# Kernel optimization log

Measured on AMD Instinct MI355X. Metric: run time of the kernel, lower is better.

The kernel has to match this reference:

```python
import jax, jax.numpy as jnp
import numpy as np

N_HEADS, D_K, D_MODEL = 16, 64, 1024
B, S = 2, 2048


def setup_inputs() -> dict:
    key = jax.random.key(0)
    ks = jax.random.split(key, 9)
    scale = 1.0 / np.sqrt(D_MODEL)
    cscale = 1.0 / np.sqrt(N_HEADS * D_K)
    return {
        "x": jax.random.normal(ks[0], (B, S, D_MODEL), dtype=jnp.float32),
        # per-head projection weights, stacked over heads: [H, d_model, d_k]
        "Wq": jax.random.uniform(ks[1], (N_HEADS, D_MODEL, D_K), jnp.float32, -scale, scale),
        "bq": jax.random.uniform(ks[2], (N_HEADS, D_K), jnp.float32, -scale, scale),
        "Wk": jax.random.uniform(ks[3], (N_HEADS, D_MODEL, D_K), jnp.float32, -scale, scale),
        "bk": jax.random.uniform(ks[4], (N_HEADS, D_K), jnp.float32, -scale, scale),
        "Wv": jax.random.uniform(ks[5], (N_HEADS, D_MODEL, D_K), jnp.float32, -scale, scale),
        "bv": jax.random.uniform(ks[6], (N_HEADS, D_K), jnp.float32, -scale, scale),
        # concat projection: [H*d_k, d_model]
        "Wc": jax.random.uniform(ks[7], (N_HEADS * D_K, D_MODEL), jnp.float32, -cscale, cscale),
        "bc": jax.random.uniform(ks[8], (D_MODEL,), jnp.float32, -cscale, cscale),
    }


def reference(x, Wq, bq, Wk, bk, Wv, bv, Wc, bc):
    # Per-head projections, vectorized across heads: [B,H,S,d_k]
    q = jnp.einsum("bsd,hdk->bhsk", x, Wq) + bq[None, :, None, :]
    k = jnp.einsum("bsd,hdk->bhsk", x, Wk) + bk[None, :, None, :]
    v = jnp.einsum("bsd,hdk->bhsk", x, Wv) + bv[None, :, None, :]
    # scores: [B,H,Sq,Skv]
    scores = jnp.einsum("bhsk,bhtk->bhst", q, k) / jnp.sqrt(jnp.asarray(D_K, x.dtype))
    # FAITHFUL to original: softmax over dim=1 of [B,S,S] = the QUERY axis (axis 2 here)
    attn = jax.nn.softmax(scores, axis=2)
    out = jnp.einsum("bhst,bhtk->bhsk", attn, v)  # [B,H,S,d_k]
    # concat heads along feature dim: [B,S,H*d_k]
    cat = jnp.transpose(out, (0, 2, 1, 3)).reshape(x.shape[0], x.shape[1], -1)
    return cat @ Wc + bc
```

## Files before the change

kernel.cpp:

```cpp
#include <hip/hip_runtime.h>
#include <hip/hip_bf16.h>

#define NH 16
#define DK 64
#define DM 1024
#define BB 2
#define SS 2048
#define BS (BB*SS)

typedef __attribute__((ext_vector_type(8))) short bf16x8;
typedef __attribute__((ext_vector_type(4))) short short4v;
typedef __attribute__((ext_vector_type(4))) float f32x4;

#define MFMA16 __builtin_amdgcn_mfma_f32_16x16x32_bf16

#if __has_builtin(__builtin_amdgcn_exp2f)
#define EXP2(x) __builtin_amdgcn_exp2f(x)
#else
#define EXP2(x) __expf((x) * 0.6931471805599453f)
#endif

static __device__ __forceinline__ float bf2f(short s) {
  union { unsigned u; float f; } v;
  v.u = ((unsigned)(unsigned short)s) << 16;
  return v.f;
}
static __device__ __forceinline__ short f2bf(float f) {
  union { float f; unsigned u; } v; v.f = f;
  unsigned r = (v.u + 0x7fffu + ((v.u >> 16) & 1u)) >> 16;
  return (short)r;
}
static __device__ __forceinline__ unsigned pkbf(float a, float b) {
  __hip_bfloat162 h = __float22bfloat162_rn(make_float2(a, b));
  union { __hip_bfloat162 h; unsigned u; } c; c.h = h; return c.u;
}

template<int C16>
static __device__ __forceinline__ int soff(int row, int chunk) {
  return row*(C16*8) + ((chunk ^ (row & (C16-1))) << 3);
}

template<int C16, int R>
static __device__ __forceinline__ void stage(const short* __restrict__ g, int gstride,
                                             short* l, int wave, int lane) {
  const int rloc = lane / C16;
  const int c    = lane % C16;
#pragma unroll
  for (int rr = 0; rr < R; rr += 4*(64/C16)) {
    int rbase = rr + wave*(64/C16);
    int row   = rbase + rloc;
    int cg    = c ^ (row & (C16-1));
    __builtin_amdgcn_global_load_lds(
        (const __attribute__((address_space(1))) void*)(g + (size_t)row*gstride + cg*8),
        (__attribute__((address_space(3))) void*)(l + rbase*(C16*8)),
        16, 0, 0);
  }
}

static __device__ __forceinline__ int permK(int r) {
  return ((r >> 5) << 5) | ((((r >> 2) & 3)) << 3) | (((r >> 4) & 1) << 2) | (r & 3);
}
template<int R>
static __device__ __forceinline__ void stageP(const short* __restrict__ g, int gstride,
                                              short* l, int wave, int lane) {
  const int rloc = lane >> 3;
  const int c    = lane & 7;
#pragma unroll
  for (int rr = 0; rr < R; rr += 32) {
    int rbase = rr + wave*8;
    int row   = rbase + rloc;
    int cg    = c ^ (row & 7);
    __builtin_amdgcn_global_load_lds(
        (const __attribute__((address_space(1))) void*)(g + (size_t)permK(row)*gstride + cg*8),
        (__attribute__((address_space(3))) void*)(l + rbase*64),
        16, 0, 0);
  }
}

__global__ __launch_bounds__(256) void k_convert(
    const float* __restrict__ x,
    const float* __restrict__ Wq, const float* __restrict__ Wk,
    const float* __restrict__ Wv, const float* __restrict__ Wc,
    short* __restrict__ xb, short* __restrict__ Wt, short* __restrict__ Wct) {
  __shared__ float T[64][65];
  const int tid = threadIdx.x;
  int bx = blockIdx.x;
  const int XB = BS*DM/(256*4);
  if (bx < XB) {
    int i = (bx*256 + tid)*4;
    float4 v = *(const float4*)&x[i];
    union { unsigned u[2]; short4v s; } o;
    o.u[0] = pkbf(v.x, v.y); o.u[1] = pkbf(v.z, v.w);
    *(short4v*)&xb[i] = o.s;
    return;
  }
  bx -= XB;
  if (bx < 48*16) {
    int th = bx >> 4, d0 = (bx & 15) * 64;
    int type = th >> 4, h = th & 15;
    const float* W = ((type == 0) ? Wq : (type == 1) ? Wk : Wv)
                     + (size_t)h*DM*DK + (size_t)d0*DK;
#pragma unroll
    for (int p = 0; p < 4; p++) {
      int dr = p*16 + (tid >> 4), dkc = (tid & 15) * 4;
      float4 v = *(const float4*)&W[(size_t)dr*DK + dkc];
      T[dkc+0][dr]=v.x; T[dkc+1][dr]=v.y; T[dkc+2][dr]=v.z; T[dkc+3][dr]=v.w;
    }
    __syncthreads();
#pragma unroll
    for (int e = 0; e < 2; e++) {
      int c = tid*2 + e, dk = c >> 3, dd = (c & 7) * 8;
      union { short s[8]; int4 v; } u;
#pragma unroll
      for (int j = 0; j < 8; j++) u.s[j] = f2bf(T[dk][dd+j]);
      *(int4*)&Wt[((size_t)th*DK + dk)*DM + d0 + dd] = u.v;
    }
    return;
  }
  bx -= 48*16;
  int n0 = (bx >> 4) * 64, k0 = (bx & 15) * 64;
#pragma unroll
  for (int p = 0; p < 4; p++) {
    int kr = p*16 + (tid >> 4), nc = (tid & 15) * 4;
    float4 v = *(const float4*)&Wc[(size_t)(k0+kr)*DM + n0 + nc];
    T[nc+0][kr]=v.x; T[nc+1][kr]=v.y; T[nc+2][kr]=v.z; T[nc+3][kr]=v.w;
  }
  __syncthreads();
#pragma unroll
  for (int e = 0; e < 2; e++) {
    int c = tid*2 + e, n = c >> 3, kk = (c & 7) * 8;
    union { short s[8]; int4 v; } u;
#pragma unroll
    for (int j = 0; j < 8; j++) u.s[j] = f2bf(T[n][kk+j]);
    *(int4*)&Wct[(size_t)(n0+n)*DM + k0 + kk] = u.v;
  }
}

__global__ __launch_bounds__(256) void k_qkv(
    const short* __restrict__ xb, const short* __restrict__ Wt,
    const float* __restrict__ bq, const float* __restrict__ bk,
    const float* __restrict__ bv,
    short* __restrict__ Qb, short* __restrict__ Kb, short* __restrict__ Vb) {
  __shared__ __align__(16) short smem[128*130];
  short* As = smem;
  short* Bs = smem + 8192;
  const int tid = threadIdx.x, wave = tid >> 6, lane = tid & 63;
  const int l15 = lane & 15, quad = lane >> 4;
  const int id = blockIdx.x, xcd = id & 7, j = id >> 3;
  const int m0 = (xcd*4 + (j & 3)) * 128, n0 = (j >> 2) * 128;
  const int mw = (wave & 1) * 64, nw = (wave >> 1) * 64;
  f32x4 acc[4][4] = {};
  for (int k0 = 0; k0 < DM; k0 += 64) {
    stage<8,128>(xb + (size_t)m0*DM + k0, DM, As, wave, lane);
    stage<8,128>(Wt + (size_t)n0*DM + k0, DM, Bs, wave, lane);
    __syncthreads();
#pragma unroll
    for (int ks = 0; ks < 2; ks++) {
      bf16x8 a[4], b[4];
#pragma unroll
      for (int g = 0; g < 4; g++)  a[g]  = *(const bf16x8*)&As[soff<8>(mw + g*16 + l15,  ks*4 + quad)];
#pragma unroll
      for (int nf = 0; nf < 4; nf++) b[nf] = *(const bf16x8*)&Bs[soff<8>(nw + nf*16 + l15, ks*4 + quad)];
#pragma unroll
      for (int g = 0; g < 4; g++)
#pragma unroll
        for (int nf = 0; nf < 4; nf++)
          acc[g][nf] = MFMA16(a[g], b[nf], acc[g][nf], 0, 0, 0);
    }
    __syncthreads();
  }
  const int th = (n0 + nw) >> 6;
  const int type = th >> 4, h = th & 15;
  const float* bias = ((type == 0) ? bq : (type == 1) ? bk : bv) + h*DK;
  const float scale = (type == 0) ? 0.18033688011112042f : 1.0f;
#pragma unroll
  for (int nf = 0; nf < 4; nf++) {
    float bval = bias[nf*16 + l15];
#pragma unroll
    for (int g = 0; g < 4; g++)
#pragma unroll
      for (int r = 0; r < 4; r++)
        smem[(mw + g*16 + quad*4 + r)*130 + nw + nf*16 + l15] =
            f2bf((acc[g][nf][r] + bval) * scale);
  }
  __syncthreads();
  const int row = tid >> 1, half = tid & 1;
  const int th2 = (n0 >> 6) + half;
  const int type2 = th2 >> 4, h2 = th2 & 15;
  short* dst = (type2 == 0) ? Qb : (type2 == 1) ? Kb : Vb;
  const int m = m0 + row, b_ = m >> 11, s = m & (SS-1);
  short* drow = dst + (size_t)((b_*NH + h2)*SS + s)*DK;
  const short* crow = smem + row*130 + half*64;
#pragma unroll
  for (int c8 = 0; c8 < 8; c8++)
    *(int4*)&drow[c8*8] = *(const int4*)&crow[c8*8];
}

__global__ __launch_bounds__(256) void k_stats(
    const short* __restrict__ Qb, const short* __restrict__ Kb,
    const short* __restrict__ Vb, short* __restrict__ Vt) {
  __shared__ __align__(16) short smem[3*8192];
  __shared__ float red[4][64];
  __shared__ float zinv[128];
  short* Ks = smem;
  const int tid = threadIdx.x, wave = tid >> 6, lane = tid & 63;
  const int l15 = lane & 15, quad = lane >> 4;
  const int id = blockIdx.x, xcd = id & 7, j = id >> 3;
  const int bh = xcd*4 + (j & 3), t0 = (j >> 2) * 128;
  const short* Qg = Qb + (size_t)bh * SS * DK;
  const short* Kg = Kb + (size_t)bh * SS * DK;
  const int mw = (wave & 1) * 64, nw = (wave >> 1) * 64;
  stage<8,128>(Kg + (size_t)t0*DK, DK, Ks, wave, lane);
  stage<8,128>(Qg, DK, smem + 8192, wave, lane);
  __syncthreads();
  bf16x8 kf[2][4];
#pragma unroll
  for (int ks = 0; ks < 2; ks++)
#pragma unroll
    for (int nf = 0; nf < 4; nf++)
      kf[ks][nf] = *(const bf16x8*)&Ks[soff<8>(nw + nf*16 + l15, ks*4 + quad)];
  float csum[4] = {0.f, 0.f, 0.f, 0.f};
  for (int it = 0; it < SS/128; it++) {
    if (it + 1 < SS/128)
      stage<8,128>(Qg + (size_t)(it+1)*128*DK, DK,
                   smem + 8192 + (((it+1) & 1) << 13), wave, lane);
    const short* Qs = smem + 8192 + ((it & 1) << 13);
    f32x4 acc[4][4] = {};
#pragma unroll
    for (int ks = 0; ks < 2; ks++) {
      bf16x8 a[4];
#pragma unroll
      for (int g = 0; g < 4; g++) a[g] = *(const bf16x8*)&Qs[soff<8>(mw + g*16 + l15, ks*4 + quad)];
#pragma unroll
      for (int g = 0; g < 4; g++)
#pragma unroll
        for (int nf = 0; nf < 4; nf++)
          acc[g][nf] = MFMA16(a[g], kf[ks][nf], acc[g][nf], 0, 0, 0);
    }
#pragma unroll
    for (int nf = 0; nf < 4; nf++)
#pragma unroll
      for (int g = 0; g < 4; g++)
#pragma unroll
        for (int r = 0; r < 4; r++)
          csum[nf] += EXP2(acc[g][nf][r]);
    __syncthreads();
  }
#pragma unroll
  for (int nf = 0; nf < 4; nf++) {
    csum[nf] += __shfl_xor(csum[nf], 16, 64);
    csum[nf] += __shfl_xor(csum[nf], 32, 64);
  }
  if (lane < 16) {
#pragma unroll
    for (int nf = 0; nf < 4; nf++) red[wave][nf*16 + lane] = csum[nf];
  }
  __syncthreads();
  if (tid < 128) {
    int half = tid >> 6, c = tid & 63;
    zinv[tid] = 1.0f / (red[half*2][c] + red[half*2 + 1][c]);
  }
  __syncthreads();
  short* Vtile = smem + 8192;
  const short* Vg = Vb + (size_t)bh * SS * DK;
#pragma unroll
  for (int it = 0; it < 4; it++) {
    int c = tid + it*256;
    int trow = c >> 3, c8 = (c & 7) * 8;
    union { int4 v; short s[8]; } u;
    u.v = *(const int4*)&Vg[(size_t)(t0 + trow)*DK + c8];
    float sc = zinv[trow];
#pragma unroll
    for (int jj = 0; jj < 8; jj++) {
      int dk = c8 + jj;
      Vtile[dk*128 + (((trow >> 3) ^ (dk & 15)) << 3) + (trow & 7)] = f2bf(bf2f(u.s[jj]) * sc);
    }
  }
  __syncthreads();
  short* Vtg = Vt + (size_t)bh * DK * SS;
#pragma unroll
  for (int it = 0; it < 4; it++) {
    int row = it*16 + (tid >> 4), cc = tid & 15;
    *(int4*)&Vtg[(size_t)row*SS + t0 + cc*8] = *(const int4*)&Vtile[soff<16>(row, cc)];
  }
}

__global__ __launch_bounds__(256, 2) void k_attnpv(
    const short* __restrict__ Qb, const short* __restrict__ Kb,
    const short* __restrict__ Vt, short* __restrict__ catg) {
  __shared__ __align__(16) short smem[32768];
  const int tid = threadIdx.x, wave = tid >> 6, lane = tid & 63;
  const int l15 = lane & 15, quad = lane >> 4;
  const int id = blockIdx.x, xcd = id & 7, jj = id >> 3;
  const int bh = xcd*4 + (jj & 3), s0 = (jj >> 2) * 128;
  const int b = bh >> 4, h = bh & 15;
  const short* Qg  = Qb + (size_t)bh * SS * DK;
  const short* Kg  = Kb + (size_t)bh * SS * DK;
  const short* Vtg = Vt + (size_t)bh * DK * SS;
  const int th_ = wave & 1, sh = wave >> 1;
  stage<8,128>(Qg + (size_t)s0*DK, DK, smem + 8192, wave, lane);
  stageP<128>(Kg, DK, smem, wave, lane);
  stage<16,64>(Vtg, SS, smem + 16384, wave, lane);
  __syncthreads();
  bf16x8 qf[2][4];
#pragma unroll
  for (int ks = 0; ks < 2; ks++)
#pragma unroll
    for (int nf = 0; nf < 4; nf++)
      qf[ks][nf] = *(const bf16x8*)&smem[8192 + soff<8>(sh*64 + nf*16 + l15, ks*4 + quad)];
  __syncthreads();
  f32x4 out[4][4] = {};
  for (int it = 0; it < SS/128; it++) {
    const short* Ks = smem + ((it & 1) << 13);
    const short* Vs = smem + 16384 + ((it & 1) << 13);
    f32x4 sacc[4][4] = {};
#pragma unroll
    for (int ks = 0; ks < 2; ks++) {
      bf16x8 a[4];
#pragma unroll
      for (int g = 0; g < 4; g++)
        a[g] = *(const bf16x8*)&Ks[soff<8>(th_*64 + g*16 + l15, ks*4 + quad)];
#pragma unroll
      for (int g = 0; g < 4; g++)
#pragma unroll
        for (int nf = 0; nf < 4; nf++)
          sacc[g][nf] = MFMA16(a[g], qf[ks][nf], sacc[g][nf], 0, 0, 0);
    }
    bf16x8 pa[4][2];
#pragma unroll
    for (int G = 0; G < 2; G++)
#pragma unroll
      for (int nf = 0; nf < 4; nf++) {
        union { unsigned u[4]; bf16x8 s8; } pu;
        pu.u[0] = pkbf(EXP2(sacc[2*G][nf][0]),   EXP2(sacc[2*G][nf][1]));
        pu.u[1] = pkbf(EXP2(sacc[2*G][nf][2]),   EXP2(sacc[2*G][nf][3]));
        pu.u[2] = pkbf(EXP2(sacc[2*G+1][nf][0]), EXP2(sacc[2*G+1][nf][1]));
        pu.u[3] = pkbf(EXP2(sacc[2*G+1][nf][2]), EXP2(sacc[2*G+1][nf][3]));
        pa[nf][G] = pu.s8;
      }
    if (it + 1 < SS/128) {
      stageP<128>(Kg + (size_t)(it+1)*128*DK, DK, smem + (((it+1) & 1) << 13), wave, lane);
      stage<16,64>(Vtg + (it+1)*128, SS, smem + 16384 + (((it+1) & 1) << 13), wave, lane);
    }
#pragma unroll
    for (int G = 0; G < 2; G++) {
      bf16x8 vb[4];
#pragma unroll
      for (int nv = 0; nv < 4; nv++)
        vb[nv] = *(const bf16x8*)&Vs[soff<16>(nv*16 + l15, 8*th_ + 4*G + quad)];
#pragma unroll
      for (int nf = 0; nf < 4; nf++)
#pragma unroll
        for (int nv = 0; nv < 4; nv++)
          out[nf][nv] = MFMA16(pa[nf][G], vb[nv], out[nf][nv], 0, 0, 0);
    }
    __syncthreads();
  }
  float* Pf = (float*)smem;
  if (th_) {
#pragma unroll
    for (int nf = 0; nf < 4; nf++)
#pragma unroll
      for (int nv = 0; nv < 4; nv++)
#pragma unroll
        for (int r = 0; r < 4; r++)
          Pf[sh*4096 + (nf*16 + quad*4 + r)*64 + nv*16 + l15] = out[nf][nv][r];
  }
  __syncthreads();
  if (!th_) {
#pragma unroll
    for (int nf = 0; nf < 4; nf++)
#pragma unroll
      for (int nv = 0; nv < 4; nv++)
#pragma unroll
        for (int r = 0; r < 4; r++) {
          float v = out[nf][nv][r] + Pf[sh*4096 + (nf*16 + quad*4 + r)*64 + nv*16 + l15];
          int s = s0 + sh*64 + nf*16 + quad*4 + r;
          catg[(size_t)(b*SS + s)*DM + h*DK + nv*16 + l15] = f2bf(v);
        }
  }
}

__global__ __launch_bounds__(256) void k_final(
    const short* __restrict__ catg, const short* __restrict__ Wct,
    const float* __restrict__ bc, float* __restrict__ out) {
  __shared__ __align__(16) short As[128*64];
  __shared__ __align__(16) short Bs[128*64];
  const int tid = threadIdx.x, wave = tid >> 6, lane = tid & 63;
  const int l15 = lane & 15, quad = lane >> 4;
  const int id = blockIdx.x, xcd = id & 7, j = id >> 3;
  const int m0 = (xcd*4 + (j & 3)) * 128, n0 = (j >> 2) * 128;
  const int mw = (wave & 1) * 64, nw = (wave >> 1) * 64;
  f32x4 acc[4][4] = {};
  for (int k0 = 0; k0 < DM; k0 += 64) {
    stage<8,128>(catg + (size_t)m0*DM + k0, DM, As, wave, lane);
    stage<8,128>(Wct  + (size_t)n0*DM + k0, DM, Bs, wave, lane);
    __syncthreads();
#pragma unroll
    for (int ks = 0; ks < 2; ks++) {
      bf16x8 a[4], b[4];
#pragma unroll
      for (int g = 0; g < 4; g++)  a[g]  = *(const bf16x8*)&As[soff<8>(mw + g*16 + l15,  ks*4 + quad)];
#pragma unroll
      for (int nf = 0; nf < 4; nf++) b[nf] = *(const bf16x8*)&Bs[soff<8>(nw + nf*16 + l15, ks*4 + quad)];
#pragma unroll
      for (int g = 0; g < 4; g++)
#pragma unroll
        for (int nf = 0; nf < 4; nf++)
          acc[g][nf] = MFMA16(a[g], b[nf], acc[g][nf], 0, 0, 0);
    }
    __syncthreads();
  }
#pragma unroll
  for (int nf = 0; nf < 4; nf++) {
    int n = n0 + nw + nf*16 + l15;
    float bval = bc[n];
#pragma unroll
    for (int g = 0; g < 4; g++)
#pragma unroll
      for (int r = 0; r < 4; r++) {
        int m = m0 + mw + g*16 + quad*4 + r;
        out[(size_t)m*DM + n] = acc[g][nf][r] + bval;
      }
  }
}

extern "C" void kernel_launch(void* const* d_in, const int* in_sizes, int n_in,
                              void* d_out, int out_size, void* d_ws, size_t ws_size,
                              hipStream_t stream) {
  (void)in_sizes; (void)n_in; (void)out_size; (void)ws_size;
  const float* x  = (const float*)d_in[0];
  const float* Wq = (const float*)d_in[1];
  const float* bq = (const float*)d_in[2];
  const float* Wk = (const float*)d_in[3];
  const float* bk = (const float*)d_in[4];
  const float* Wv = (const float*)d_in[5];
  const float* bv = (const float*)d_in[6];
  const float* Wc = (const float*)d_in[7];
  const float* bc = (const float*)d_in[8];
  float* out = (float*)d_out;

  char* ws = (char*)d_ws;
  size_t o = 0;
  short* xb  = (short*)(ws + o); o += (size_t)BS*DM*2;
  short* Wt  = (short*)(ws + o); o += (size_t)3*NH*DK*DM*2;
  short* Wct = (short*)(ws + o); o += (size_t)DM*DM*2;
  short* Qb  = (short*)(ws + o); o += (size_t)BB*NH*SS*DK*2;
  short* Kb  = (short*)(ws + o); o += (size_t)BB*NH*SS*DK*2;
  short* Vb  = (short*)(ws + o); o += (size_t)BB*NH*SS*DK*2;
  short* Vt  = (short*)(ws + o); o += (size_t)BB*NH*DK*SS*2;
  short* cat = (short*)(ws + o); o += (size_t)BS*DM*2;

  const int nconv = BS*DM/(256*4) + 48*16 + 256;
  k_convert<<<dim3(nconv), 256, 0, stream>>>(x, Wq, Wk, Wv, Wc, xb, Wt, Wct);
  k_qkv   <<<dim3(768), 256, 0, stream>>>(xb, Wt, bq, bk, bv, Qb, Kb, Vb);
  k_stats <<<dim3(512), 256, 0, stream>>>(Qb, Kb, Vb, Vt);
  k_attnpv<<<dim3(512), 256, 0, stream>>>(Qb, Kb, Vt, cat);
  k_final <<<dim3(256), 256, 0, stream>>>(cat, Wct, bc, out);
}
```

Baseline: 220.2 us.

## Double-buffer LDS tiles in QKV and output projection GEMMs

The QKV and final projection GEMM kernels now use two LDS buffers per operand. Each iteration stages the next K-slice into one buffer while MFMAs read the current one, with a single barrier per iteration. The goal is to hide global-load latency behind compute. The QKV epilogue also drops the LDS transpose and writes bf16 results straight to global memory, which removes a barrier but produces 2-byte scattered stores instead of 16-byte vector stores. LDS use per block doubles to 64 KB, which may reduce occupancy.

After: 205.0 us. 6.9% less time.

```diff
diff --git a/kernel.cpp b/kernel.cpp
--- a/kernel.cpp
+++ b/kernel.cpp
@@ -141,19 +141,25 @@
     const float* __restrict__ bq, const float* __restrict__ bk,
     const float* __restrict__ bv,
     short* __restrict__ Qb, short* __restrict__ Kb, short* __restrict__ Vb) {
-  __shared__ __align__(16) short smem[128*130];
-  short* As = smem;
-  short* Bs = smem + 8192;
+  __shared__ __align__(16) short smem[32768];
   const int tid = threadIdx.x, wave = tid >> 6, lane = tid & 63;
   const int l15 = lane & 15, quad = lane >> 4;
   const int id = blockIdx.x, xcd = id & 7, j = id >> 3;
   const int m0 = (xcd*4 + (j & 3)) * 128, n0 = (j >> 2) * 128;
   const int mw = (wave & 1) * 64, nw = (wave >> 1) * 64;
+  const short* Ag = xb + (size_t)m0*DM;
+  const short* Bg = Wt + (size_t)n0*DM;
+  stage<8,128>(Ag, DM, smem, wave, lane);
+  stage<8,128>(Bg, DM, smem + 16384, wave, lane);
+  __syncthreads();
   f32x4 acc[4][4] = {};
-  for (int k0 = 0; k0 < DM; k0 += 64) {
-    stage<8,128>(xb + (size_t)m0*DM + k0, DM, As, wave, lane);
-    stage<8,128>(Wt + (size_t)n0*DM + k0, DM, Bs, wave, lane);
-    __syncthreads();
+  for (int it = 0; it < DM/64; it++) {
+    if (it + 1 < DM/64) {
+      stage<8,128>(Ag + (it+1)*64, DM, smem + (((it+1) & 1) << 13), wave, lane);
+      stage<8,128>(Bg + (it+1)*64, DM, smem + 16384 + (((it+1) & 1) << 13), wave, lane);
+    }
+    const short* As = smem + ((it & 1) << 13);
+    const short* Bs = smem + 16384 + ((it & 1) << 13);
 #pragma unroll
     for (int ks = 0; ks < 2; ks++) {
       bf16x8 a[4], b[4];
@@ -171,29 +177,22 @@
   }
   const int th = (n0 + nw) >> 6;
   const int type = th >> 4, h = th & 15;
+  short* dst = (type == 0) ? Qb : (type == 1) ? Kb : Vb;
   const float* bias = ((type == 0) ? bq : (type == 1) ? bk : bv) + h*DK;
   const float scale = (type == 0) ? 0.18033688011112042f : 1.0f;
 #pragma unroll
   for (int nf = 0; nf < 4; nf++) {
-    float bval = bias[nf*16 + l15];
+    int dk = nf*16 + l15;
+    float bval = bias[dk];
 #pragma unroll
     for (int g = 0; g < 4; g++)
 #pragma unroll
-      for (int r = 0; r < 4; r++)
-        smem[(mw + g*16 + quad*4 + r)*130 + nw + nf*16 + l15] =
-            f2bf((acc[g][nf][r] + bval) * scale);
-  }
-  __syncthreads();
-  const int row = tid >> 1, half = tid & 1;
-  const int th2 = (n0 >> 6) + half;
-  const int type2 = th2 >> 4, h2 = th2 & 15;
-  short* dst = (type2 == 0) ? Qb : (type2 == 1) ? Kb : Vb;
-  const int m = m0 + row, b_ = m >> 11, s = m & (SS-1);
-  short* drow = dst + (size_t)((b_*NH + h2)*SS + s)*DK;
-  const short* crow = smem + row*130 + half*64;
-#pragma unroll
-  for (int c8 = 0; c8 < 8; c8++)
-    *(int4*)&drow[c8*8] = *(const int4*)&crow[c8*8];
+      for (int r = 0; r < 4; r++) {
+        int m = m0 + mw + g*16 + quad*4 + r;
+        int b_ = m >> 11, s = m & (SS-1);
+        dst[(size_t)((b_*NH + h)*SS + s)*DK + dk] = f2bf((acc[g][nf][r] + bval) * scale);
+      }
+  }
 }
 
 __global__ __launch_bounds__(256) void k_stats(
@@ -384,18 +383,25 @@
 __global__ __launch_bounds__(256) void k_final(
     const short* __restrict__ catg, const short* __restrict__ Wct,
     const float* __restrict__ bc, float* __restrict__ out) {
-  __shared__ __align__(16) short As[128*64];
-  __shared__ __align__(16) short Bs[128*64];
+  __shared__ __align__(16) short smem[32768];
   const int tid = threadIdx.x, wave = tid >> 6, lane = tid & 63;
   const int l15 = lane & 15, quad = lane >> 4;
   const int id = blockIdx.x, xcd = id & 7, j = id >> 3;
   const int m0 = (xcd*4 + (j & 3)) * 128, n0 = (j >> 2) * 128;
   const int mw = (wave & 1) * 64, nw = (wave >> 1) * 64;
+  const short* Ag = catg + (size_t)m0*DM;
+  const short* Bg = Wct  + (size_t)n0*DM;
+  stage<8,128>(Ag, DM, smem, wave, lane);
+  stage<8,128>(Bg, DM, smem + 16384, wave, lane);
+  __syncthreads();
   f32x4 acc[4][4] = {};
-  for (int k0 = 0; k0 < DM; k0 += 64) {
-    stage<8,128>(catg + (size_t)m0*DM + k0, DM, As, wave, lane);
-    stage<8,128>(Wct  + (size_t)n0*DM + k0, DM, Bs, wave, lane);
-    __syncthreads();
+  for (int it = 0; it < DM/64; it++) {
+    if (it + 1 < DM/64) {
+      stage<8,128>(Ag + (it+1)*64, DM, smem + (((it+1) & 1) << 13), wave, lane);
+      stage<8,128>(Bg + (it+1)*64, DM, smem + 16384 + (((it+1) & 1) << 13), wave, lane);
+    }
+    const short* As = smem + ((it & 1) << 13);
+    const short* Bs = smem + 16384 + ((it & 1) << 13);
 #pragma unroll
     for (int ks = 0; ks < 2; ks++) {
       bf16x8 a[4], b[4];
```
